# Performance work log

Measured on AMD Instinct MI355X. Metric: run time of the kernel, lower is better.

The kernel has to match this reference:

```python
import jax, jax.numpy as jnp
import numpy as np

T, D, E, F = 8192, 1024, 8, 3584


def setup_inputs() -> dict:
    key = jax.random.key(0)
    ks = jax.random.split(key, 5)
    scale_in = 1.0 / np.sqrt(D)
    scale_ff = 1.0 / np.sqrt(F)
    return {
        "x": jax.random.normal(ks[0], (T, D), dtype=jnp.float32),
        "w1": jax.random.normal(ks[1], (E, F, D), dtype=jnp.float32) * scale_in,
        "w3": jax.random.normal(ks[2], (E, F, D), dtype=jnp.float32) * scale_in,
        "w2": jax.random.normal(ks[3], (E, D, F), dtype=jnp.float32) * scale_ff,
        "router_logits": jax.random.normal(ks[4], (T, E), dtype=jnp.float32),
        "top_k": 2,
    }


def reference(x, w1, w3, w2, router_logits, top_k):
    # Routing: softmax over experts, keep top-k, renormalize (Mixtral, normalize=True)
    probs = jax.nn.softmax(router_logits, axis=-1)            # [T, E]
    top_vals, top_idx = jax.lax.top_k(probs, top_k)           # [T, k]
    top_vals = top_vals / jnp.sum(top_vals, axis=-1, keepdims=True)
    tokens = jnp.arange(x.shape[0])[:, None]
    weights = jnp.zeros_like(probs).at[tokens, top_idx].set(top_vals)  # [T, E]

    gate = jnp.einsum('td,efd->tef', x, w1)                   # [T, E, F]
    up = jnp.einsum('td,efd->tef', x, w3)                     # [T, E, F]
    h = jax.nn.silu(gate) * up                                # [T, E, F]
    out = jnp.einsum('te,tef,edf->td', weights, h, w2)        # [T, D]
    return out
```

## Files before the change

kernel.cpp:

```cpp
#include <hip/hip_runtime.h>
#include <cstdint>

#define T_TOK 8192
#define D_DIM 1024
#define E_EXP 8
#define F_DIM 3584
#define NROW  (2 * T_TOK)
#define PROWS_PAD 18432
#define MAXTILES 72
#define MAXBANDS 18

typedef __attribute__((ext_vector_type(8))) __bf16 bf16x8;
typedef __attribute__((ext_vector_type(4))) float f32x4;

__device__ __forceinline__ void gload16(const void* g, void* l) {
    __builtin_amdgcn_global_load_lds(
        (const __attribute__((address_space(1))) void*)(g),
        (__attribute__((address_space(3))) void*)(l),
        16, 0, 0);
}

__global__ void cvt_kernel(const float* __restrict__ in, __bf16* __restrict__ out, long n) {
    long i = ((long)blockIdx.x * blockDim.x + threadIdx.x) * 8;
    if (i >= n) return;
    const float4 f0 = *(const float4*)(in + i);
    const float4 f1 = *(const float4*)(in + i + 4);
    bf16x8 o;
    o[0] = (__bf16)f0.x; o[1] = (__bf16)f0.y; o[2] = (__bf16)f0.z; o[3] = (__bf16)f0.w;
    o[4] = (__bf16)f1.x; o[5] = (__bf16)f1.y; o[6] = (__bf16)f1.z; o[7] = (__bf16)f1.w;
    *(bf16x8*)(out + i) = o;
}

__global__ void route_kernel(const float* __restrict__ rl, int* cnt,
                             int* __restrict__ eidx, float* __restrict__ ewgt) {
    int t = blockIdx.x * blockDim.x + threadIdx.x;
    if (t >= T_TOK) return;
    float l[8];
#pragma unroll
    for (int e = 0; e < 8; ++e) l[e] = rl[t * 8 + e];
    int i0 = 0; float v0 = l[0];
    int i1 = -1; float v1 = -1e30f;
#pragma unroll
    for (int e = 1; e < 8; ++e) {
        if (l[e] > v0) { v1 = v0; i1 = i0; v0 = l[e]; i0 = e; }
        else if (l[e] > v1) { v1 = l[e]; i1 = e; }
    }
    float wsec = 1.f / (1.f + __expf(v0 - v1));
    eidx[2 * t] = i0; eidx[2 * t + 1] = i1;
    ewgt[2 * t] = 1.f - wsec; ewgt[2 * t + 1] = wsec;
    atomicAdd(&cnt[i0], 1); atomicAdd(&cnt[i1], 1);
}

__global__ void scan_kernel(const int* __restrict__ cnt, int* __restrict__ pofs) {
    if (threadIdx.x == 0) {
        int a = 0;
        for (int e = 0; e < E_EXP; ++e) { pofs[e] = a; a += (cnt[e] + 255) & ~255; }
        pofs[E_EXP] = a;
    }
}

__global__ void tiles_kernel(const int* __restrict__ pofs, int* __restrict__ tile_e,
                             int* __restrict__ tile_r0, int* __restrict__ meta) {
    if (threadIdx.x == 0) {
        int n = 0;
        for (int e = 0; e < E_EXP; ++e)
            for (int r = pofs[e]; r < pofs[e + 1]; r += 256) {
                tile_e[n] = e; tile_r0[n] = r; ++n;
            }
        meta[0] = n;
    }
}

__global__ void assign_kernel(const int* __restrict__ eidx, const int* __restrict__ pofs,
                              int* cnt2, int* __restrict__ tokOf, int* __restrict__ rowOf) {
    int t = blockIdx.x * blockDim.x + threadIdx.x;
    if (t >= T_TOK) return;
#pragma unroll
    for (int s = 0; s < 2; ++s) {
        int e = eidx[2 * t + s];
        int pos = atomicAdd(&cnt2[e], 1);
        int prow = pofs[e] + pos;
        tokOf[prow] = t;
        rowOf[2 * t + s] = prow;
    }
}

__global__ void gather_kernel(const float* __restrict__ x, const int* __restrict__ tokOf,
                              __bf16* __restrict__ xg) {
    const int idx = blockIdx.x * blockDim.x + threadIdx.x;
    const int pr = idx >> 7;
    const int j = (idx & 127) * 8;
    const int tk = tokOf[pr];
    bf16x8 o = {};
    if (tk >= 0) {
        const float4 f0 = *(const float4*)(x + (long)tk * D_DIM + j);
        const float4 f1 = *(const float4*)(x + (long)tk * D_DIM + j + 4);
        o[0] = (__bf16)f0.x; o[1] = (__bf16)f0.y; o[2] = (__bf16)f0.z; o[3] = (__bf16)f0.w;
        o[4] = (__bf16)f1.x; o[5] = (__bf16)f1.y; o[6] = (__bf16)f1.z; o[7] = (__bf16)f1.w;
    }
    *(bf16x8*)(xg + (long)pr * D_DIM + j) = o;
}

__device__ __forceinline__ int chunk_row(int c) { return ((c >> 7) << 4) | ((c >> 2) & 15); }
__device__ __forceinline__ int chunk_col(int c) {
    return ((c >> 6) & 1) * 32 + (((c & 3) * 8) ^ (((c >> 5) & 1) << 4));
}

template <int NT>
__device__ __forceinline__ void moe_pipeline(
    const __bf16* const (&srcA)[2][2], const __bf16* const (&srcB)[2][2],
    __bf16 (&Ash)[2][2][8192], __bf16 (&Bsh)[2][2][8192],
    int wave, int abase, int wm, int bh, int bsel, f32x4 (&acc)[8][4])
{
    auto stA = [&](int buf, int kt, int h) {
        const long k0 = (long)kt * 64;
        gload16(srcA[h][0] + k0, &Ash[buf][h][(0 * 512 + wave * 64) * 8]);
        gload16(srcA[h][1] + k0, &Ash[buf][h][(1 * 512 + wave * 64) * 8]);
    };
    auto stB = [&](int buf, int kt, int h) {
        const long k0 = (long)kt * 64;
        gload16(srcB[h][0] + k0, &Bsh[buf][h][(0 * 512 + wave * 64) * 8]);
        gload16(srcB[h][1] + k0, &Bsh[buf][h][(1 * 512 + wave * 64) * 8]);
    };

    bf16x8 bfr[4][2];
    bf16x8 a0, a1, a2, a3;

#define LD_A(Ab, q) \
    a0 = *(const bf16x8*)((Ab) + ((2*(q)) * 2 + 0) * 512); \
    a1 = *(const bf16x8*)((Ab) + ((2*(q)) * 2 + 1) * 512); \
    a2 = *(const bf16x8*)((Ab) + ((2*(q)+1) * 2 + 0) * 512); \
    a3 = *(const bf16x8*)((Ab) + ((2*(q)+1) * 2 + 1) * 512);

#define LD_B(Bb) \
    _Pragma("unroll") for (int ni = 0; ni < 4; ++ni) { \
        bfr[ni][0] = *(const bf16x8*)((Bb) + ((bsel * 4 + ni) * 2 + 0) * 512); \
        bfr[ni][1] = *(const bf16x8*)((Bb) + ((bsel * 4 + ni) * 2 + 1) * 512); \
    }

#define MFMA_Q(q) \
    _Pragma("unroll") for (int ni = 0; ni < 4; ++ni) { \
        acc[2*(q)][ni]   = __builtin_amdgcn_mfma_f32_16x16x32_bf16(a0, bfr[ni][0], acc[2*(q)][ni], 0, 0, 0); \
        acc[2*(q)][ni]   = __builtin_amdgcn_mfma_f32_16x16x32_bf16(a1, bfr[ni][1], acc[2*(q)][ni], 0, 0, 0); \
        acc[2*(q)+1][ni] = __builtin_amdgcn_mfma_f32_16x16x32_bf16(a2, bfr[ni][0], acc[2*(q)+1][ni], 0, 0, 0); \
        acc[2*(q)+1][ni] = __builtin_amdgcn_mfma_f32_16x16x32_bf16(a3, bfr[ni][1], acc[2*(q)+1][ni], 0, 0, 0); \
    }

#define PH_OPEN() \
    __builtin_amdgcn_sched_barrier(0); \
    __builtin_amdgcn_s_barrier(); \
    asm volatile("s_waitcnt lgkmcnt(0)" ::: "memory"); \
    __builtin_amdgcn_sched_barrier(0); \
    __builtin_amdgcn_s_setprio(1);

#define PH_CLOSE() \
    __builtin_amdgcn_s_setprio(0); \
    __builtin_amdgcn_sched_barrier(0); \
    __builtin_amdgcn_s_barrier(); \
    __builtin_amdgcn_sched_barrier(0);

#define PH_CLOSE_G(lastf) \
    __builtin_amdgcn_s_setprio(0); \
    __builtin_amdgcn_sched_barrier(0); \
    if (lastf) { asm volatile("s_waitcnt vmcnt(0)" ::: "memory"); } \
    else       { asm volatile("s_waitcnt vmcnt(4)" ::: "memory"); } \
    __builtin_amdgcn_s_barrier(); \
    __builtin_amdgcn_sched_barrier(0);

    stA(0, 0, 0); stA(0, 0, 1); stB(0, 0, 0); stB(0, 0, 1);
    stB(1, 1, 0); stB(1, 1, 1);
    asm volatile("s_waitcnt vmcnt(4)" ::: "memory");
    __builtin_amdgcn_s_barrier();

    const __bf16* AbE = &Ash[0][wm][abase];
    const __bf16* BbE = &Bsh[0][bh][abase];
    const __bf16* AbO = &Ash[1][wm][abase];
    const __bf16* BbO = &Bsh[1][bh][abase];

    for (int it = 0; it < NT / 2; ++it) {
        const int kv = 2 * it + 1;
        const bool last = (it == NT / 2 - 1);
        LD_A(AbE, 0) LD_B(BbE)
        stA(1, kv, 0);
        PH_OPEN() MFMA_Q(0) PH_CLOSE()
        LD_A(AbE, 1)
        stA(1, kv, 1);
        PH_OPEN() MFMA_Q(1) PH_CLOSE()
        LD_A(AbE, 2)
        if (!last) stB(0, kv + 1, 0);
        PH_OPEN() MFMA_Q(2) PH_CLOSE()
        LD_A(AbE, 3)
        if (!last) stB(0, kv + 1, 1);
        PH_OPEN() MFMA_Q(3) PH_CLOSE_G(last)
        LD_A(AbO, 0) LD_B(BbO)
        if (!last) stA(0, kv + 1, 0);
        PH_OPEN() MFMA_Q(0) PH_CLOSE()
        LD_A(AbO, 1)
        if (!last) stA(0, kv + 1, 1);
        PH_OPEN() MFMA_Q(1) PH_CLOSE()
        LD_A(AbO, 2)
        if (!last) stB(1, kv + 2, 0);
        PH_OPEN() MFMA_Q(2) PH_CLOSE()
        LD_A(AbO, 3)
        if (!last) stB(1, kv + 2, 1);
        PH_OPEN() MFMA_Q(3) PH_CLOSE_G(last)
    }
#undef LD_A
#undef LD_B
#undef MFMA_Q
#undef PH_OPEN
#undef PH_CLOSE
#undef PH_CLOSE_G
}

__global__ __launch_bounds__(512, 1)
void gemm1_kernel(const __bf16* __restrict__ xg,
                  const __bf16* __restrict__ w1b,
                  const __bf16* __restrict__ w3b,
                  const int* __restrict__ tile_e,
                  const int* __restrict__ tile_r0,
                  const int* __restrict__ meta,
                  __bf16* __restrict__ h) {
    const int count = meta[0];
    const int bands = (count + 3) >> 2;
    const int live = bands * 112;
    const int bid = blockIdx.x;
    if (bid >= live) return;
    const int w = (bid & 7) * (live >> 3) + (bid >> 3);
    const int q28 = w / 28, r = w % 28;
    const int tile = (q28 >> 2) * 4 + r / 7;
    const int nt = (q28 & 3) * 7 + r % 7;
    if (tile >= count) return;
    const int e = tile_e[tile];
    const int row0 = tile_r0[tile];

    __shared__ __align__(16) __bf16 Ash[2][2][8192];
    __shared__ __align__(16) __bf16 Bsh[2][2][8192];

    const int tid = threadIdx.x;
    const int wave = tid >> 6, lane = tid & 63;
    const int wm = wave >> 2, wn = wave & 3;
    const int fr = lane & 15, fg = lane >> 4;

    const __bf16* srcA[2][2];
    const __bf16* srcB[2][2];
#pragma unroll
    for (int half = 0; half < 2; ++half)
#pragma unroll
        for (int j = 0; j < 2; ++j) {
            const int c = tid + j * 512;
            srcA[half][j] = xg + (long)(row0 + half * 128 + chunk_row(c)) * D_DIM + chunk_col(c);
            const int rb = half * 128 + chunk_row(c);
            const int blk = rb >> 4;
            const int f = nt * 128 + (blk >> 1) * 16 + (rb & 15);
            srcB[half][j] = ((blk & 1) ? w3b : w1b) + ((long)e * F_DIM + f) * D_DIM + chunk_col(c);
        }

    const int abase = fr * 32 + ((fg * 8) ^ ((fr & 8) << 1));
    f32x4 acc[8][4] = {};

    moe_pipeline<16>(srcA, srcB, Ash, Bsh, wave, abase, wm, wn >> 1, wn & 1, acc);

#pragma unroll
    for (int mi = 0; mi < 8; ++mi) {
#pragma unroll
        for (int reg = 0; reg < 4; ++reg) {
            const int lm = wm * 128 + mi * 16 + fg * 4 + reg;
            const long hrow = (long)(row0 + lm) * F_DIM;
#pragma unroll
            for (int b = 0; b < 2; ++b) {
                const float g = acc[mi][2 * b][reg];
                const float u = acc[mi][2 * b + 1][reg];
                const float s = g / (1.f + __expf(-g));
                h[hrow + nt * 128 + (wn * 2 + b) * 16 + fr] = (__bf16)(s * u);
            }
        }
    }
}

__global__ __launch_bounds__(512, 1)
void gemm2_kernel(const __bf16* __restrict__ hb,
                  const __bf16* __restrict__ w2b,
                  const int* __restrict__ tile_e,
                  const int* __restrict__ tile_r0,
                  const int* __restrict__ meta,
                  __bf16* __restrict__ o2p) {
    const int count = meta[0];
    const int bands = (count + 3) >> 2;
    const int live = bands * 32;
    const int bid = blockIdx.x;
    if (bid >= live) return;
    const int w = (bid & 7) * (live >> 3) + (bid >> 3);
    const int band = w >> 5, s = w & 31;
    const int tile = band * 4 + (s >> 3);
    const int nt = s & 3, ks = (s >> 2) & 1;
    if (tile >= count) return;
    const int e = tile_e[tile];
    const int row0 = tile_r0[tile];

    __shared__ __align__(16) __bf16 Ash[2][2][8192];
    __shared__ __align__(16) __bf16 Bsh[2][2][8192];

    const int tid = threadIdx.x;
    const int wave = tid >> 6, lane = tid & 63;
    const int wm = wave >> 2, wn = wave & 3;
    const int fr = lane & 15, fg = lane >> 4;
    const int kofs = ks * (F_DIM / 2);

    const __bf16* srcA[2][2];
    const __bf16* srcB[2][2];
#pragma unroll
    for (int half = 0; half < 2; ++half)
#pragma unroll
        for (int j = 0; j < 2; ++j) {
            const int c = tid + j * 512;
            srcA[half][j] = hb + (long)(row0 + half * 128 + chunk_row(c)) * F_DIM + kofs + chunk_col(c);
            const int rb = half * 128 + chunk_row(c);
            srcB[half][j] = w2b + ((long)e * D_DIM + nt * 256 + rb) * F_DIM + kofs + chunk_col(c);
        }

    const int abase = fr * 32 + ((fg * 8) ^ ((fr & 8) << 1));
    f32x4 acc[8][4] = {};

    moe_pipeline<28>(srcA, srcB, Ash, Bsh, wave, abase, wm, wn >> 1, wn & 1, acc);

    __bf16* ps = o2p + (long)ks * PROWS_PAD * D_DIM;
#pragma unroll
    for (int mi = 0; mi < 8; ++mi) {
#pragma unroll
        for (int reg = 0; reg < 4; ++reg) {
            const int lm = wm * 128 + mi * 16 + fg * 4 + reg;
            const long obase = (long)(row0 + lm) * D_DIM + nt * 256 + wn * 64 + fr;
#pragma unroll
            for (int ni = 0; ni < 4; ++ni)
                ps[obase + ni * 16] = (__bf16)acc[mi][ni][reg];
        }
    }
}

__global__ void combine_kernel(const __bf16* __restrict__ o2p, const int* __restrict__ rowOf,
                               const float* __restrict__ ewgt, float* __restrict__ out) {
    const int idx = blockIdx.x * blockDim.x + threadIdx.x;
    const int t = idx >> 7;
    const int j = (idx & 127) * 8;
    const long r0 = rowOf[2 * t], r1 = rowOf[2 * t + 1];
    const float w0 = ewgt[2 * t], w1 = ewgt[2 * t + 1];
    float r[8] = {0, 0, 0, 0, 0, 0, 0, 0};
#pragma unroll
    for (int s = 0; s < 2; ++s) {
        const bf16x8 a = *(const bf16x8*)(o2p + ((long)s * PROWS_PAD + r0) * D_DIM + j);
        const bf16x8 b = *(const bf16x8*)(o2p + ((long)s * PROWS_PAD + r1) * D_DIM + j);
#pragma unroll
        for (int q = 0; q < 8; ++q) r[q] += w0 * (float)a[q] + w1 * (float)b[q];
    }
    float4* ob = (float4*)(out + (long)t * D_DIM + j);
    ob[0] = make_float4(r[0], r[1], r[2], r[3]);
    ob[1] = make_float4(r[4], r[5], r[6], r[7]);
}

extern "C" void kernel_launch(void* const* d_in, const int* in_sizes, int n_in,
                              void* d_out, int out_size, void* d_ws, size_t ws_size,
                              hipStream_t stream) {
    const float* x  = (const float*)d_in[0];
    const float* w1 = (const float*)d_in[1];
    const float* w3 = (const float*)d_in[2];
    const float* w2 = (const float*)d_in[3];
    const float* rl = (const float*)d_in[4];
    float* out = (float*)d_out;

    char* ws = (char*)d_ws;
    size_t off = 0;
    auto alloc = [&](size_t bytes) {
        void* p = ws + off;
        off += (bytes + 255) & ~(size_t)255;
        return p;
    };
    __bf16* xg   = (__bf16*)alloc((size_t)PROWS_PAD * D_DIM * 2);
    __bf16* w1b  = (__bf16*)alloc((size_t)E_EXP * F_DIM * D_DIM * 2);
    __bf16* w3b  = (__bf16*)alloc((size_t)E_EXP * F_DIM * D_DIM * 2);
    __bf16* hbuf = (__bf16*)alloc((size_t)PROWS_PAD * F_DIM * 2);
    int*   tokOf = (int*)alloc(PROWS_PAD * 4);
    int*   rowOf = (int*)alloc(NROW * 4);
    int*   eidx  = (int*)alloc(NROW * 4);
    float* ewgt  = (float*)alloc(NROW * 4);
    int*   cnt1  = (int*)alloc(64);
    int*   cnt2  = (int*)alloc(64);
    int*   pofs  = (int*)alloc(64);
    int*   tileE = (int*)alloc(MAXTILES * 4 + 64);
    int*   tileR = (int*)alloc(MAXTILES * 4 + 64);
    int*   meta  = (int*)alloc(64);
    __bf16* w2b = (__bf16*)ws;
    __bf16* o2p = (__bf16*)(ws + (size_t)E_EXP * D_DIM * F_DIM * 2);

    hipMemsetAsync(cnt1, 0, 64, stream);
    hipMemsetAsync(cnt2, 0, 64, stream);
    hipMemsetAsync(tokOf, 0xFF, PROWS_PAD * 4, stream);

    route_kernel<<<T_TOK / 256, 256, 0, stream>>>(rl, cnt1, eidx, ewgt);
    scan_kernel<<<1, 64, 0, stream>>>(cnt1, pofs);
    tiles_kernel<<<1, 64, 0, stream>>>(pofs, tileE, tileR, meta);
    assign_kernel<<<T_TOK / 256, 256, 0, stream>>>(eidx, pofs, cnt2, tokOf, rowOf);
    gather_kernel<<<PROWS_PAD * 128 / 256, 256, 0, stream>>>(x, tokOf, xg);

    {
        const long n = (long)E_EXP * F_DIM * D_DIM;
        const int blks = (int)(n / 8 / 256);
        cvt_kernel<<<blks, 256, 0, stream>>>(w1, w1b, n);
        cvt_kernel<<<blks, 256, 0, stream>>>(w3, w3b, n);
    }

    gemm1_kernel<<<MAXBANDS * 112, 512, 0, stream>>>(xg, w1b, w3b, tileE, tileR, meta, hbuf);

    {
        const long n = (long)E_EXP * D_DIM * F_DIM;
        cvt_kernel<<<(int)(n / 8 / 256), 256, 0, stream>>>(w2, w2b, n);
    }

    gemm2_kernel<<<MAXBANDS * 32, 512, 0, stream>>>(hbuf, w2b, tileE, tileR, meta, o2p);

    combine_kernel<<<T_TOK * (D_DIM / 8) / 256, 256, 0, stream>>>(o2p, rowOf, ewgt, out);
}
```

Baseline: 695.5 us.

## Make both expert GEMM kernels persistent with atomic work-stealing tile queue

Both grouped GEMM kernels now launch a fixed grid of 256 blocks. Each block repeatedly grabs the next work item from a global atomic counter instead of mapping one block to one tile. This targets launch overhead and tail imbalance from the oversized, data-dependent grids. The trade-off is that it drops the previous XCD-aware block-to-work swizzle, which may change L2 locality. The early `continue` path can also race on the shared work index, since no barrier protects it before it is rewritten.

```diff
diff --git a/kernel.cpp b/kernel.cpp
--- a/kernel.cpp
+++ b/kernel.cpp
@@ -220,59 +220,64 @@
                   const int* __restrict__ tile_e,
                   const int* __restrict__ tile_r0,
                   const int* __restrict__ meta,
+                  int* __restrict__ tick,
                   __bf16* __restrict__ h) {
     const int count = meta[0];
     const int bands = (count + 3) >> 2;
     const int live = bands * 112;
-    const int bid = blockIdx.x;
-    if (bid >= live) return;
-    const int w = (bid & 7) * (live >> 3) + (bid >> 3);
-    const int q28 = w / 28, r = w % 28;
-    const int tile = (q28 >> 2) * 4 + r / 7;
-    const int nt = (q28 & 3) * 7 + r % 7;
-    if (tile >= count) return;
-    const int e = tile_e[tile];
-    const int row0 = tile_r0[tile];
-
-    __shared__ __align__(16) __bf16 Ash[2][2][8192];
-    __shared__ __align__(16) __bf16 Bsh[2][2][8192];
+    __shared__ int s_w;
 
     const int tid = threadIdx.x;
     const int wave = tid >> 6, lane = tid & 63;
     const int wm = wave >> 2, wn = wave & 3;
     const int fr = lane & 15, fg = lane >> 4;
-
-    const __bf16* srcA[2][2];
-    const __bf16* srcB[2][2];
-#pragma unroll
-    for (int half = 0; half < 2; ++half)
-#pragma unroll
-        for (int j = 0; j < 2; ++j) {
-            const int c = tid + j * 512;
-            srcA[half][j] = xg + (long)(row0 + half * 128 + chunk_row(c)) * D_DIM + chunk_col(c);
-            const int rb = half * 128 + chunk_row(c);
-            const int blk = rb >> 4;
-            const int f = nt * 128 + (blk >> 1) * 16 + (rb & 15);
-            srcB[half][j] = ((blk & 1) ? w3b : w1b) + ((long)e * F_DIM + f) * D_DIM + chunk_col(c);
-        }
-
     const int abase = fr * 32 + ((fg * 8) ^ ((fr & 8) << 1));
-    f32x4 acc[8][4] = {};
-
-    moe_pipeline<16>(srcA, srcB, Ash, Bsh, wave, abase, wm, wn >> 1, wn & 1, acc);
-
-#pragma unroll
-    for (int mi = 0; mi < 8; ++mi) {
-#pragma unroll
-        for (int reg = 0; reg < 4; ++reg) {
-            const int lm = wm * 128 + mi * 16 + fg * 4 + reg;
-            const long hrow = (long)(row0 + lm) * F_DIM;
-#pragma unroll
-            for (int b = 0; b < 2; ++b) {
-                const float g = acc[mi][2 * b][reg];
-                const float u = acc[mi][2 * b + 1][reg];
-                const float s = g / (1.f + __expf(-g));
-                h[hrow + nt * 128 + (wn * 2 + b) * 16 + fr] = (__bf16)(s * u);
+
+    __shared__ __align__(16) __bf16 Ash[2][2][8192];
+    __shared__ __align__(16) __bf16 Bsh[2][2][8192];
+
+    for (;;) {
+        if (tid == 0) s_w = atomicAdd(tick, 1);
+        __syncthreads();
+        const int w = s_w;
+        if (w >= live) break;
+        const int q28 = w / 28, r = w % 28;
+        const int tile = (q28 >> 2) * 4 + r / 7;
+        const int nt = (q28 & 3) * 7 + r % 7;
+        if (tile >= count) continue;
+        const int e = tile_e[tile];
+        const int row0 = tile_r0[tile];
+
+        const __bf16* srcA[2][2];
+        const __bf16* srcB[2][2];
+#pragma unroll
+        for (int half = 0; half < 2; ++half)
+#pragma unroll
+            for (int j = 0; j < 2; ++j) {
+                const int c = tid + j * 512;
+                srcA[half][j] = xg + (long)(row0 + half * 128 + chunk_row(c)) * D_DIM + chunk_col(c);
+                const int rb = half * 128 + chunk_row(c);
+                const int blk = rb >> 4;
+                const int f = nt * 128 + (blk >> 1) * 16 + (rb & 15);
+                srcB[half][j] = ((blk & 1) ? w3b : w1b) + ((long)e * F_DIM + f) * D_DIM + chunk_col(c);
+            }
+
+        f32x4 acc[8][4] = {};
+        moe_pipeline<16>(srcA, srcB, Ash, Bsh, wave, abase, wm, wn >> 1, wn & 1, acc);
+
+#pragma unroll
+        for (int mi = 0; mi < 8; ++mi) {
+#pragma unroll
+            for (int reg = 0; reg < 4; ++reg) {
+                const int lm = wm * 128 + mi * 16 + fg * 4 + reg;
+                const long hrow = (long)(row0 + lm) * F_DIM;
+#pragma unroll
+                for (int b = 0; b < 2; ++b) {
+                    const float g = acc[mi][2 * b][reg];
+                    const float u = acc[mi][2 * b + 1][reg];
+                    const float s = g / (1.f + __expf(-g));
+                    h[hrow + nt * 128 + (wn * 2 + b) * 16 + fr] = (__bf16)(s * u);
+                }
             }
         }
     }
@@ -284,56 +289,61 @@
                   const int* __restrict__ tile_e,
                   const int* __restrict__ tile_r0,
                   const int* __restrict__ meta,
+                  int* __restrict__ tick,
                   __bf16* __restrict__ o2p) {
     const int count = meta[0];
     const int bands = (count + 3) >> 2;
     const int live = bands * 32;
-    const int bid = blockIdx.x;
-    if (bid >= live) return;
-    const int w = (bid & 7) * (live >> 3) + (bid >> 3);
-    const int band = w >> 5, s = w & 31;
-    const int tile = band * 4 + (s >> 3);
-    const int nt = s & 3, ks = (s >> 2) & 1;
-    if (tile >= count) return;
-    const int e = tile_e[tile];
-    const int row0 = tile_r0[tile];
-
-    __shared__ __align__(16) __bf16 Ash[2][2][8192];
-    __shared__ __align__(16) __bf16 Bsh[2][2][8192];
+    __shared__ int s_w;
 
     const int tid = threadIdx.x;
     const int wave = tid >> 6, lane = tid & 63;
     const int wm = wave >> 2, wn = wave & 3;
     const int fr = lane & 15, fg = lane >> 4;
-    const int kofs = ks * (F_DIM / 2);
-
-    const __bf16* srcA[2][2];
-    const __bf16* srcB[2][2];
-#pragma unroll
-    for (int half = 0; half < 2; ++half)
-#pragma unroll
-        for (int j = 0; j < 2; ++j) {
-            const int c = tid + j * 512;
-            srcA[half][j] = hb + (long)(row0 + half * 128 + chunk_row(c)) * F_DIM + kofs + chunk_col(c);
-            const int rb = half * 128 + chunk_row(c);
-            srcB[half][j] = w2b + ((long)e * D_DIM + nt * 256 + rb) * F_DIM + kofs + chunk_col(c);
-        }
-
     const int abase = fr * 32 + ((fg * 8) ^ ((fr & 8) << 1));
-    f32x4 acc[8][4] = {};
-
-    moe_pipeline<28>(srcA, srcB, Ash, Bsh, wave, abase, wm, wn >> 1, wn & 1, acc);
-
-    __bf16* ps = o2p + (long)ks * PROWS_PAD * D_DIM;
-#pragma unroll
-    for (int mi = 0; mi < 8; ++mi) {
-#pragma unroll
-        for (int reg = 0; reg < 4; ++reg) {
-            const int lm = wm * 128 + mi * 16 + fg * 4 + reg;
-            const long obase = (long)(row0 + lm) * D_DIM + nt * 256 + wn * 64 + fr;
-#pragma unroll
-            for (int ni = 0; ni < 4; ++ni)
-                ps[obase + ni * 16] = (__bf16)acc[mi][ni][reg];
+
+    __shared__ __align__(16) __bf16 Ash[2][2][8192];
+    __shared__ __align__(16) __bf16 Bsh[2][2][8192];
+
+    for (;;) {
+        if (tid == 0) s_w = atomicAdd(tick, 1);
+        __syncthreads();
+        const int w = s_w;
+        if (w >= live) break;
+        const int band = w >> 5, s = w & 31;
+        const int tile = band * 4 + (s >> 3);
+        const int nt = s & 3, ks = (s >> 2) & 1;
+        if (tile >= count) continue;
+        const int e = tile_e[tile];
+        const int row0 = tile_r0[tile];
+        const int kofs = ks * (F_DIM / 2);
+
+        const __bf16* srcA[2][2];
+        const __bf16* srcB[2][2];
+#pragma unroll
+        for (int half = 0; half < 2; ++half)
+#pragma unroll
+            for (int j = 0; j < 2; ++j) {
+                const int c = tid + j * 512;
+                srcA[half][j] = hb + (long)(row0 + half * 128 + chunk_row(c)) * F_DIM + kofs + chunk_col(c);
+                const int rb = half * 128 + chunk_row(c);
+                srcB[half][j] = w2b + ((long)e * D_DIM + nt * 256 + rb) * F_DIM + kofs + chunk_col(c);
+            }
+
+        f32x4 acc[8][4] = {};
+        moe_pipeline<28>(srcA, srcB, Ash, Bsh, wave, abase, wm, wn >> 1, wn & 1, acc);
+
+        __bf16* ps = o2p + (long)ks * PROWS_PAD * D_DIM;
+#pragma unroll
+        for (int mi = 0; mi < 8; ++mi) {
+#pragma unroll
+            for (int reg = 0; reg < 4; ++reg) {
+                const int lm = wm * 128 + mi * 16 + fg * 4 + reg;
+                const long obase = (long)(row0 + lm) * D_DIM + nt * 256 + wn * 64 + fr;
+#pragma unroll
+                for (int ni = 0; ni < 4; ++ni)
+                    ps[obase + ni * 16] = (__bf16)acc[mi][ni][reg];
+            }
         }
     }
 }
@@ -389,11 +399,13 @@
     int*   tileE = (int*)alloc(MAXTILES * 4 + 64);
     int*   tileR = (int*)alloc(MAXTILES * 4 + 64);
     int*   meta  = (int*)alloc(64);
+    int*   ticks = (int*)alloc(64);
     __bf16* w2b = (__bf16*)ws;
     __bf16* o2p = (__bf16*)(ws + (size_t)E_EXP * D_DIM * F_DIM * 2);
 
     hipMemsetAsync(cnt1, 0, 64, stream);
     hipMemsetAsync(cnt2, 0, 64, stream);
+    hipMemsetAsync(ticks, 0, 64, stream);
     hipMemsetAsync(tokOf, 0xFF, PROWS_PAD * 4, stream);
 
     route_kernel<<<T_TOK / 256, 256, 0, stream>>>(rl, cnt1, eidx, ewgt);
@@ -409,14 +421,14 @@
         cvt_kernel<<<blks, 256, 0, stream>>>(w3, w3b, n);
     }
 
-    gemm1_kernel<<<MAXBANDS * 112, 512, 0, stream>>>(xg, w1b, w3b, tileE, tileR, meta, hbuf);
+    gemm1_kernel<<<256, 512, 0, stream>>>(xg, w1b, w3b, tileE, tileR, meta, &ticks[0], hbuf);
 
     {
         const long n = (long)E_EXP * D_DIM * F_DIM;
         cvt_kernel<<<(int)(n / 8 / 256), 256, 0, stream>>>(w2, w2b, n);
     }
 
-    gemm2_kernel<<<MAXBANDS * 32, 512, 0, stream>>>(hbuf, w2b, tileE, tileR, meta, o2p);
+    gemm2_kernel<<<256, 512, 0, stream>>>(hbuf, w2b, tileE, tileR, meta, &ticks[1], o2p);
 
     combine_kernel<<<T_TOK * (D_DIM / 8) / 256, 256, 0, stream>>>(o2p, rowOf, ewgt, out);
 }
```

Measured after the change: 712.1 us. 2.4% more time.
